# Optimization experiments

Hardware: AMD Instinct MI355X
Metric: run time of the kernel (lower is better)

The kernel has to match this reference:

```python
import jax, jax.numpy as jnp
import numpy as np

B, S, D, H = 2, 2048, 1024, 16
DK = D // H


def setup_inputs() -> dict:
    key = jax.random.key(0)
    ks = jax.random.split(key, 9)
    scale = 1.0 / np.sqrt(D)
    inp = {
        "x": jax.random.normal(ks[0], (B, S, D), dtype=jnp.float32),
        "mask": jnp.triu(jnp.ones((S, S), dtype=jnp.int32), k=1),  # 1 = masked (causal)
        "Wq": jax.random.normal(ks[1], (D, D), dtype=jnp.float32) * scale,
        "bq": jnp.zeros((D,), dtype=jnp.float32),
        "Wk": jax.random.normal(ks[2], (D, D), dtype=jnp.float32) * scale,
        "bk": jnp.zeros((D,), dtype=jnp.float32),
        "Wv": jax.random.normal(ks[3], (D, D), dtype=jnp.float32) * scale,
        "bv": jnp.zeros((D,), dtype=jnp.float32),
        "Wo": jax.random.normal(ks[4], (D, D), dtype=jnp.float32) * scale,
        "bo": jnp.zeros((D,), dtype=jnp.float32),
    }
    return inp


def reference(x, mask, Wq, bq, Wk, bk, Wv, bv, Wo, bo):
    # Linear projections (torch nn.Linear: x @ W.T + b; here W stored as (D, D) in
    # (in, out) layout so x @ W + b is equivalent math).
    q = x @ Wq + bq  # (B, S, D)
    k = x @ Wk + bk
    v = x @ Wv + bv
    # Split heads: (B, S, D) -> (B, H, S, DK)
    def split(t):
        return t.reshape(B, S, H, DK).transpose(0, 2, 1, 3)
    q, k, v = split(q), split(k), split(v)
    # Scaled dot-product attention with full score matrix (faithful to original)
    scores = jnp.einsum("bhsd,bhtd->bhst", q, k) / jnp.sqrt(jnp.float32(DK))
    scores = jnp.where(mask[None, None, :, :] == 1, -jnp.inf, scores)
    attn = jax.nn.softmax(scores, axis=-1)  # (B, H, S, S)
    out = jnp.einsum("bhst,bhtd->bhsd", attn, v)
    # Merge heads and final projection
    out = out.transpose(0, 2, 1, 3).reshape(B, S, D)
    return out @ Wo + bo
```

## Files before the change

kernel.cpp:

```cpp
#include <hip/hip_runtime.h>
#include <hip/hip_bf16.h>
#include <cstdint>
#include <cstddef>

typedef __attribute__((ext_vector_type(8))) short short8;
typedef __attribute__((ext_vector_type(4))) float f32x4;
typedef __attribute__((ext_vector_type(4))) unsigned int u32x4;
typedef unsigned short u16;
typedef unsigned int u32;

#define NB 2
#define NS 2048
#define ND 1024
#define NH 16
#define NDK 64

__device__ __forceinline__ u16 f2bf(float f){
  u32 u = __builtin_bit_cast(u32, f);
  u += 0x7fffu + ((u >> 16) & 1u);
  return (u16)(u >> 16);
}

__device__ __forceinline__ u32 pk2(float lo, float hi){
  return (u32)f2bf(lo) | ((u32)f2bf(hi) << 16);
}

__device__ __forceinline__ u32 cvtpk(float lo, float hi){
  u32 r;
  asm("v_cvt_pk_bf16_f32 %0, %1, %2" : "=v"(r) : "v"(lo), "v"(hi));
  return r;
}

__device__ __forceinline__ void stage16(const u16* g, u16* l, int lane){
#if defined(__has_builtin) && __has_builtin(__builtin_amdgcn_global_load_lds)
  __builtin_amdgcn_global_load_lds(
      (const __attribute__((address_space(1))) u32*)(const void*)g,
      (__attribute__((address_space(3))) u32*)(void*)l, 16, 0, 0);
#else
  ((uint4*)l)[lane] = *(const uint4*)g;
#endif
}


__global__ __launch_bounds__(256) void prep_kernel(
    const float* __restrict__ Wq, const float* __restrict__ Wk,
    const float* __restrict__ Wv, const float* __restrict__ Wo,
    const float* __restrict__ x,
    u16* __restrict__ Wt, u16* __restrict__ xb)
{
  const int z = blockIdx.z;
  const int tx = threadIdx.x, ty = threadIdx.y;
  if (z == 4){
    const int base = ((blockIdx.y*32 + (int)blockIdx.x)*256 + ty*32 + tx)*16;
    float4 v0 = *(const float4*)(x+base);
    float4 v1 = *(const float4*)(x+base+4);
    float4 v2 = *(const float4*)(x+base+8);
    float4 v3 = *(const float4*)(x+base+12);
    const int blk = base & ~31;
    const int h4  = (base & 16) ? 4 : 0;
    *(uint2*)(xb + blk +  0 + h4) = make_uint2(pk2(v0.x,v0.y), pk2(v0.z,v0.w));
    *(uint2*)(xb + blk +  8 + h4) = make_uint2(pk2(v1.x,v1.y), pk2(v1.z,v1.w));
    *(uint2*)(xb + blk + 16 + h4) = make_uint2(pk2(v2.x,v2.y), pk2(v2.z,v2.w));
    *(uint2*)(xb + blk + 24 + h4) = make_uint2(pk2(v3.x,v3.y), pk2(v3.z,v3.w));
    return;
  }
  const float* W = (z==0)?Wq:(z==1)?Wk:(z==2)?Wv:Wo;
  u16* dst = Wt + (size_t)z*ND*ND;
  __shared__ float t[32][33];
  const int n0 = blockIdx.x*32, k0 = blockIdx.y*32;
  const int ptx = 8*((tx&15)>>2) + (tx&3) + 4*(tx>>4);
#pragma unroll
  for (int i=0;i<4;i++) t[ty+i*8][tx] = W[(size_t)(k0+ty+i*8)*ND + n0+tx];
  __syncthreads();
#pragma unroll
  for (int i=0;i<4;i++) dst[(size_t)(n0+ty+i*8)*ND + k0+ptx] = f2bf(t[tx][ty+i*8]);
}

template<int MODE>
__global__ __launch_bounds__(256,3) void gemm_kernel(
    const u16* __restrict__ Abf, const u16* __restrict__ Wtz,
    const float* __restrict__ bias0, const float* __restrict__ bias1, const float* __restrict__ bias2,
    u16* __restrict__ Qout, u16* __restrict__ Kout, u16* __restrict__ Vtout,
    float* __restrict__ Fout)
{
  int bx, by;
  if constexpr (MODE==0){
    const int f  = blockIdx.x;
    const int fp = (f & 7)*96 + (f >> 3);
    by = fp / 24; bx = fp % 24;
  } else { bx = blockIdx.x; by = blockIdx.y; }
  const int tid  = threadIdx.x;
  const int lane = tid & 63;
  const int wv   = tid >> 6;
  const int a = lane & 15, g = lane >> 4;
  const int wm = wv >> 1, wn = wv & 1;
  const int m0 = by * 128, n0 = bx * 128;
  const int z  = (MODE==0) ? (n0 >> 10) : 0;

  __shared__ u16 Al[128*64];
  __shared__ u16 Bl[128*64];

  f32x4 acc[4][4] = {};

  const int grow = lane >> 3;
  const int gcol = (lane & 7) * 8;

#pragma unroll 1
  for (int k0 = 0; k0 < ND; k0 += 64) {
    __syncthreads();
#pragma unroll
    for (int i=0;i<4;++i){
      const int r = 32*wv + 8*i + grow;
      const int cs = gcol ^ ((r&7)<<3);
      stage16(Abf + (size_t)(m0+r)*ND + k0 + cs, &Al[(32*wv+8*i)*64], lane);
      stage16(Wtz + (size_t)(n0+r)*ND + k0 + cs, &Bl[(32*wv+8*i)*64], lane);
    }
    __syncthreads();

#pragma unroll
    for (int kk=0; kk<64; kk+=32){
      short8 af[4], bfr[4];
#pragma unroll
      for (int mi=0;mi<4;++mi){
        const int rr = wm*64 + mi*16 + a;
        const int rsw = (rr&7)<<3;
        af[mi] = *(const short8*)(&Al[rr*64] + ((kk + 8*g) ^ rsw));
      }
#pragma unroll
      for (int ni=0;ni<4;++ni){
        const int rr = wn*64 + ni*16 + a;
        const int rsw = (rr&7)<<3;
        bfr[ni] = *(const short8*)(&Bl[rr*64] + ((kk + 8*g) ^ rsw));
      }
      __builtin_amdgcn_s_setprio(1);
#pragma unroll
      for (int mi=0;mi<4;++mi)
#pragma unroll
        for (int ni=0;ni<4;++ni)
          acc[mi][ni] = __builtin_amdgcn_mfma_f32_16x16x32_bf16(af[mi], bfr[ni], acc[mi][ni], 0,0,0);
      __builtin_amdgcn_s_setprio(0);
    }
  }

#pragma unroll
  for (int mi=0;mi<4;++mi){
#pragma unroll
    for (int ni=0;ni<4;++ni){
      const int n  = n0 + wn*64 + ni*16 + a;
      const int mb = m0 + wm*64 + mi*16 + 4*g;
      if constexpr (MODE==0){
        const int nn = n & 1023;
        const float* bp = (z==0)? bias0 : (z==1)? bias1 : bias2;
        const float bias = bp[nn];
        const int h = nn >> 6, dk = nn & 63;
        const int b = mb >> 11, s = mb & 2047;
        if (z==2){
          const int sb = s & 31;
          const int col = (s & ~31) + 8*((sb&15)>>2) + 4*(sb>>4);
          *(uint2*)&Vtout[(((size_t)b*NH + h)*NDK + dk)*NS + col] =
            make_uint2(pk2(acc[mi][ni][0]+bias, acc[mi][ni][1]+bias),
                       pk2(acc[mi][ni][2]+bias, acc[mi][ni][3]+bias));
        } else {
          u16* dst = (z==0)? Qout : Kout;
          const float sc = (z==0)? 0.1803368801111601f : 1.0f;
          const int d5 = dk & 31;
          const int pdk = (dk & 32) + 8*((d5&15)>>2) + (d5&3) + 4*(d5>>4);
#pragma unroll
          for (int r=0;r<4;++r)
            dst[(((size_t)b*NH + h)*NS + (s+r))*NDK + pdk] = f2bf((acc[mi][ni][r]+bias)*sc);
        }
      } else {
        const float bias = bias0[n];
#pragma unroll
        for (int r=0;r<4;++r)
          Fout[(size_t)(mb+r)*ND + n] = acc[mi][ni][r] + bias;
      }
    }
  }
}

#define KOFF(p_, q_) ((p_)*8192 + (q_)*4096)
#define VOFF(p_, q_) (16384 + (p_)*8192 + (q_)*4096)
#define FIXM 10.0f

__global__ __launch_bounds__(512,4) void attn_kernel(
    const u16* __restrict__ Qg, const u16* __restrict__ Kg,
    const u16* __restrict__ Vtg, u16* __restrict__ Og)
{
  const int tid  = threadIdx.x;
  const int lane = tid & 63, wv = tid >> 6;
  const int qw = wv & 3, par = wv >> 2;
  const int a = lane & 15, g = lane >> 4;
  const int bh = blockIdx.x;
  const int qt = blockIdx.y;
  const int qb = (qt < 8) ? qt : (23 - qt);
  const int qB  = qb * 128;
  const int q0w = qB + qw*32;
  const int nr  = qb + 1;

  __shared__ u16 SH[32768];

  short8 qf[2][2];
#pragma unroll
  for (int qi=0; qi<2; ++qi){
    const u16* qptr = Qg + ((size_t)bh*NS + q0w + qi*16 + a)*NDK;
    qf[qi][0] = *(const short8*)(qptr + 8*g);
    qf[qi][1] = *(const short8*)(qptr + 32 + 8*g);
  }

  float ls[2] = {0.f, 0.f};
  f32x4 accO[4][2] = {};

  const int srow = wv*8 + (lane >> 3);
  const int scol = (lane & 7) * 8;
  const int scs  = scol ^ ((srow & 7) << 3);
  const u16* kgp = Kg  + (size_t)bh*NS*NDK + (size_t)srow*NDK + scs;
  const u16* vgp = Vtg + (size_t)bh*NDK*NS + (size_t)srow*NS  + scs;

  stage16(kgp,            &SH[KOFF(0,0) + wv*512], lane);
  stage16(kgp + 64*NDK,   &SH[KOFF(0,1) + wv*512], lane);
  stage16(vgp,            &SH[VOFF(0,0) + wv*512], lane);
  stage16(vgp + 64,       &SH[VOFF(0,1) + wv*512], lane);
  __syncthreads();

  const u16* kstg = kgp + 128*NDK;
  const u16* vstg = vgp + 128;

  int cur = 0;
#pragma unroll 1
  for (int r=0; r<nr; ++r){
    const int t = 2*r + par;
    const int kv0 = t * 64;
    if (r+1 < nr){
      stage16(kstg,          &SH[KOFF(cur^1,0) + wv*512], lane);
      stage16(kstg + 64*NDK, &SH[KOFF(cur^1,1) + wv*512], lane);
      stage16(vstg,          &SH[VOFF(cur^1,0) + wv*512], lane);
      stage16(vstg + 64,     &SH[VOFF(cur^1,1) + wv*512], lane);
      kstg += 128*NDK; vstg += 128;
    }

    if (kv0 <= q0w + 31){
      const u16* Kb = &SH[KOFF(cur,par)];
      const u16* Vb = &SH[VOFF(cur,par)];
      f32x4 sc[2][4] = {};
      __builtin_amdgcn_s_setprio(1);
#pragma unroll
      for (int kvf=0; kvf<4; ++kvf){
        const int rr = kvf*16 + a;
        const int rsw = (rr&7)<<3;
        const u16* rp = Kb + rr*64;
        short8 kf0 = *(const short8*)(rp + ((8*g) ^ rsw));
        short8 kf1 = *(const short8*)(rp + ((32 + 8*g) ^ rsw));
#pragma unroll
        for (int qi=0; qi<2; ++qi){
          sc[qi][kvf] = __builtin_amdgcn_mfma_f32_16x16x32_bf16(kf0, qf[qi][0], sc[qi][kvf], 0,0,0);
          sc[qi][kvf] = __builtin_amdgcn_mfma_f32_16x16x32_bf16(kf1, qf[qi][1], sc[qi][kvf], 0,0,0);
        }
      }
      __builtin_amdgcn_s_setprio(0);

      const bool dm = (kv0 + 63 > q0w);
      short8 pf[2][2];
#pragma unroll
      for (int qi=0; qi<2; ++qi){
        const int q = q0w + qi*16 + a;
        if (dm){
#pragma unroll
          for (int kvf=0;kvf<4;++kvf)
#pragma unroll
            for (int rr=0;rr<4;++rr){
              const int kv = kv0 + kvf*16 + 4*g + rr;
              if (kv > q) sc[qi][kvf][rr] = -1e30f;
            }
        }
        float rsum = 0.f;
        u32 pw[2][4];
#pragma unroll
        for (int kvf=0;kvf<4;++kvf){
          const float e0 = exp2f(sc[qi][kvf][0] - FIXM);
          const float e1 = exp2f(sc[qi][kvf][1] - FIXM);
          const float e2 = exp2f(sc[qi][kvf][2] - FIXM);
          const float e3 = exp2f(sc[qi][kvf][3] - FIXM);
          rsum += (e0+e1)+(e2+e3);
          pw[kvf>>1][(kvf&1)*2+0] = cvtpk(e0,e1);
          pw[kvf>>1][(kvf&1)*2+1] = cvtpk(e2,e3);
        }
        pf[qi][0] = __builtin_bit_cast(short8, *(u32x4*)pw[0]);
        pf[qi][1] = __builtin_bit_cast(short8, *(u32x4*)pw[1]);
        rsum += __shfl_xor(rsum,16);
        rsum += __shfl_xor(rsum,32);
        ls[qi] += rsum;
      }

      __builtin_amdgcn_s_setprio(1);
#pragma unroll
      for (int dkg=0;dkg<4;++dkg){
        const int rr = dkg*16 + a;
        const int rsw = (rr&7)<<3;
        const u16* rp = Vb + rr*64;
        short8 vf0 = *(const short8*)(rp + ((8*g) ^ rsw));
        short8 vf1 = *(const short8*)(rp + ((32 + 8*g) ^ rsw));
#pragma unroll
        for (int qi=0; qi<2; ++qi){
          accO[dkg][qi] = __builtin_amdgcn_mfma_f32_16x16x32_bf16(vf0, pf[qi][0], accO[dkg][qi], 0,0,0);
          accO[dkg][qi] = __builtin_amdgcn_mfma_f32_16x16x32_bf16(vf1, pf[qi][1], accO[dkg][qi], 0,0,0);
        }
      }
      __builtin_amdgcn_s_setprio(0);
    }

    __syncthreads();
    cur ^= 1;
  }

  float* ms = (float*)SH;
  if (par == 1){
#pragma unroll
    for (int qi=0; qi<2; ++qi){
      const int idx = (((qw*64 + lane)*2) + qi)*17;
#pragma unroll
      for (int dkg=0;dkg<4;++dkg)
#pragma unroll
        for (int j=0;j<4;++j) ms[idx + dkg*4 + j] = accO[dkg][qi][j];
      ms[idx+16] = ls[qi];
    }
  }
  __syncthreads();

  if (par == 0){
    u16* Lw = &SH[18432] + qw*2048;
#pragma unroll
    for (int qi=0; qi<2; ++qi){
      const int idx = (((qw*64 + lane)*2) + qi)*17;
      const float linv = 1.0f / (ls[qi] + ms[idx+16]);
      const int row = qi*16 + a;
#pragma unroll
      for (int dkg=0; dkg<4; ++dkg){
        const int pcol = 32*(dkg>>1) + 8*g + 4*(dkg&1);
        const float o0 = (accO[dkg][qi][0] + ms[idx+dkg*4+0])*linv;
        const float o1 = (accO[dkg][qi][1] + ms[idx+dkg*4+1])*linv;
        const float o2 = (accO[dkg][qi][2] + ms[idx+dkg*4+2])*linv;
        const float o3 = (accO[dkg][qi][3] + ms[idx+dkg*4+3])*linv;
        *(uint2*)&Lw[(row<<6) + (pcol ^ ((row&7)<<3))] = make_uint2(cvtpk(o0,o1), cvtpk(o2,o3));
      }
    }
    const int b = bh >> 4, h = bh & 15;
#pragma unroll
    for (int j=0; j<4; ++j){
      const int row = j*8 + (lane>>3);
      const int cc  = (lane&7)*8;
      uint4 d = *(const uint4*)&Lw[(row<<6) + (cc ^ ((row&7)<<3))];
      *(uint4*)(Og + ((size_t)b*NS + qB + qw*32 + row)*ND + h*NDK + cc) = d;
    }
  }
}

extern "C" void kernel_launch(void* const* d_in, const int* in_sizes, int n_in,
                              void* d_out, int out_size, void* d_ws, size_t ws_size,
                              hipStream_t stream) {
  (void)in_sizes; (void)n_in; (void)out_size; (void)ws_size;
  const float* x  = (const float*)d_in[0];
  const float* Wq = (const float*)d_in[2];
  const float* bq = (const float*)d_in[3];
  const float* Wk = (const float*)d_in[4];
  const float* bk = (const float*)d_in[5];
  const float* Wv = (const float*)d_in[6];
  const float* bv = (const float*)d_in[7];
  const float* Wo = (const float*)d_in[8];
  const float* bo = (const float*)d_in[9];
  float* out = (float*)d_out;

  u16* Wt  = (u16*)d_ws;
  u16* Qb  = Wt  + (size_t)4194304;
  u16* Kb  = Qb  + (size_t)4194304;
  u16* Vtb = Kb  + (size_t)4194304;
  u16* XO  = Vtb + (size_t)4194304;

  prep_kernel<<<dim3(32,32,5), dim3(32,8,1), 0, stream>>>(Wq, Wk, Wv, Wo, x, Wt, XO);
  gemm_kernel<0><<<dim3(768), dim3(256), 0, stream>>>(
      XO, Wt, bq, bk, bv, Qb, Kb, Vtb, (float*)nullptr);
  attn_kernel<<<dim3(32,16), dim3(512), 0, stream>>>(Qb, Kb, Vtb, XO);
  gemm_kernel<1><<<dim3(8,32), dim3(256), 0, stream>>>(
      XO, Wt + (size_t)3*1048576, bo, nullptr, nullptr,
      (u16*)nullptr, (u16*)nullptr, (u16*)nullptr, out);
}
```

Baseline: 107.2 us.

## Drop KV-parity wave split in attention; use 4-wave blocks over all KV tiles

```diff
diff --git a/kernel.cpp b/kernel.cpp
--- a/kernel.cpp
+++ b/kernel.cpp
@@ -179,26 +179,24 @@
   }
 }
 
-#define KOFF(p_, q_) ((p_)*8192 + (q_)*4096)
-#define VOFF(p_, q_) (16384 + (p_)*8192 + (q_)*4096)
+#define KOFF(p_) ((p_)*4096)
+#define VOFF(p_) (8192 + (p_)*4096)
 #define FIXM 10.0f
 
-__global__ __launch_bounds__(512,4) void attn_kernel(
+__global__ __launch_bounds__(256,4) void attn_kernel(
     const u16* __restrict__ Qg, const u16* __restrict__ Kg,
     const u16* __restrict__ Vtg, u16* __restrict__ Og)
 {
   const int tid  = threadIdx.x;
   const int lane = tid & 63, wv = tid >> 6;
-  const int qw = wv & 3, par = wv >> 2;
   const int a = lane & 15, g = lane >> 4;
   const int bh = blockIdx.x;
-  const int qt = blockIdx.y;
-  const int qb = (qt < 8) ? qt : (23 - qt);
+  const int qb = 15 - (int)blockIdx.y;
   const int qB  = qb * 128;
-  const int q0w = qB + qw*32;
-  const int nr  = qb + 1;
-
-  __shared__ u16 SH[32768];
+  const int q0w = qB + wv*32;
+  const int nt  = 2*qb + 2;
+
+  __shared__ u16 SH[16384];
 
   short8 qf[2][2];
 #pragma unroll
@@ -211,37 +209,39 @@
   float ls[2] = {0.f, 0.f};
   f32x4 accO[4][2] = {};
 
-  const int srow = wv*8 + (lane >> 3);
+  const int srow = wv*16 + (lane >> 3);
   const int scol = (lane & 7) * 8;
   const int scs  = scol ^ ((srow & 7) << 3);
   const u16* kgp = Kg  + (size_t)bh*NS*NDK + (size_t)srow*NDK + scs;
   const u16* vgp = Vtg + (size_t)bh*NDK*NS + (size_t)srow*NS  + scs;
-
-  stage16(kgp,            &SH[KOFF(0,0) + wv*512], lane);
-  stage16(kgp + 64*NDK,   &SH[KOFF(0,1) + wv*512], lane);
-  stage16(vgp,            &SH[VOFF(0,0) + wv*512], lane);
-  stage16(vgp + 64,       &SH[VOFF(0,1) + wv*512], lane);
+  u16* const kd0 = &SH[(wv*16)*64];
+  u16* const kd1 = &SH[(wv*16+8)*64];
+
+  stage16(kgp,          kd0,        lane);
+  stage16(kgp + 8*NDK,  kd1,        lane);
+  stage16(vgp,          kd0 + 8192, lane);
+  stage16(vgp + 8*NS,   kd1 + 8192, lane);
   __syncthreads();
 
-  const u16* kstg = kgp + 128*NDK;
-  const u16* vstg = vgp + 128;
+  const u16* kstg = kgp + 64*NDK;
+  const u16* vstg = vgp + 64;
 
   int cur = 0;
 #pragma unroll 1
-  for (int r=0; r<nr; ++r){
-    const int t = 2*r + par;
+  for (int t=0; t<nt; ++t){
     const int kv0 = t * 64;
-    if (r+1 < nr){
-      stage16(kstg,          &SH[KOFF(cur^1,0) + wv*512], lane);
-      stage16(kstg + 64*NDK, &SH[KOFF(cur^1,1) + wv*512], lane);
-      stage16(vstg,          &SH[VOFF(cur^1,0) + wv*512], lane);
-      stage16(vstg + 64,     &SH[VOFF(cur^1,1) + wv*512], lane);
-      kstg += 128*NDK; vstg += 128;
+    if (t+1 < nt){
+      const int nb = (cur^1)*4096;
+      stage16(kstg,          kd0 + nb,        lane);
+      stage16(kstg + 8*NDK,  kd1 + nb,        lane);
+      stage16(vstg,          kd0 + nb + 8192, lane);
+      stage16(vstg + 8*NS,   kd1 + nb + 8192, lane);
+      kstg += 64*NDK; vstg += 64;
     }
 
     if (kv0 <= q0w + 31){
-      const u16* Kb = &SH[KOFF(cur,par)];
-      const u16* Vb = &SH[VOFF(cur,par)];
+      const u16* Kb = &SH[KOFF(cur)];
+      const u16* Vb = &SH[VOFF(cur)];
       f32x4 sc[2][4] = {};
       __builtin_amdgcn_s_setprio(1);
 #pragma unroll
@@ -313,45 +313,28 @@
     cur ^= 1;
   }
 
-  float* ms = (float*)SH;
-  if (par == 1){
-#pragma unroll
-    for (int qi=0; qi<2; ++qi){
-      const int idx = (((qw*64 + lane)*2) + qi)*17;
-#pragma unroll
-      for (int dkg=0;dkg<4;++dkg)
-#pragma unroll
-        for (int j=0;j<4;++j) ms[idx + dkg*4 + j] = accO[dkg][qi][j];
-      ms[idx+16] = ls[qi];
-    }
-  }
-  __syncthreads();
-
-  if (par == 0){
-    u16* Lw = &SH[18432] + qw*2048;
-#pragma unroll
-    for (int qi=0; qi<2; ++qi){
-      const int idx = (((qw*64 + lane)*2) + qi)*17;
-      const float linv = 1.0f / (ls[qi] + ms[idx+16]);
-      const int row = qi*16 + a;
-#pragma unroll
-      for (int dkg=0; dkg<4; ++dkg){
-        const int pcol = 32*(dkg>>1) + 8*g + 4*(dkg&1);
-        const float o0 = (accO[dkg][qi][0] + ms[idx+dkg*4+0])*linv;
-        const float o1 = (accO[dkg][qi][1] + ms[idx+dkg*4+1])*linv;
-        const float o2 = (accO[dkg][qi][2] + ms[idx+dkg*4+2])*linv;
-        const float o3 = (accO[dkg][qi][3] + ms[idx+dkg*4+3])*linv;
-        *(uint2*)&Lw[(row<<6) + (pcol ^ ((row&7)<<3))] = make_uint2(cvtpk(o0,o1), cvtpk(o2,o3));
-      }
-    }
-    const int b = bh >> 4, h = bh & 15;
-#pragma unroll
-    for (int j=0; j<4; ++j){
-      const int row = j*8 + (lane>>3);
-      const int cc  = (lane&7)*8;
-      uint4 d = *(const uint4*)&Lw[(row<<6) + (cc ^ ((row&7)<<3))];
-      *(uint4*)(Og + ((size_t)b*NS + qB + qw*32 + row)*ND + h*NDK + cc) = d;
-    }
+  u16* Lw = &SH[0] + wv*2048;
+#pragma unroll
+  for (int qi=0; qi<2; ++qi){
+    const float linv = 1.0f / ls[qi];
+    const int row = qi*16 + a;
+#pragma unroll
+    for (int dkg=0; dkg<4; ++dkg){
+      const int pcol = 32*(dkg>>1) + 8*g + 4*(dkg&1);
+      const float o0 = accO[dkg][qi][0]*linv;
+      const float o1 = accO[dkg][qi][1]*linv;
+      const float o2 = accO[dkg][qi][2]*linv;
+      const float o3 = accO[dkg][qi][3]*linv;
+      *(uint2*)&Lw[(row<<6) + (pcol ^ ((row&7)<<3))] = make_uint2(cvtpk(o0,o1), cvtpk(o2,o3));
+    }
+  }
+  const int b = bh >> 4, h = bh & 15;
+#pragma unroll
+  for (int j=0; j<4; ++j){
+    const int row = j*8 + (lane>>3);
+    const int cc  = (lane&7)*8;
+    uint4 d = *(const uint4*)&Lw[(row<<6) + (cc ^ ((row&7)<<3))];
+    *(uint4*)(Og + ((size_t)b*NS + qB + wv*32 + row)*ND + h*NDK + cc) = d;
   }
 }
 
@@ -379,7 +362,7 @@
   prep_kernel<<<dim3(32,32,5), dim3(32,8,1), 0, stream>>>(Wq, Wk, Wv, Wo, x, Wt, XO);
   gemm_kernel<0><<<dim3(768), dim3(256), 0, stream>>>(
       XO, Wt, bq, bk, bv, Qb, Kb, Vtb, (float*)nullptr);
-  attn_kernel<<<dim3(32,16), dim3(512), 0, stream>>>(Qb, Kb, Vtb, XO);
+  attn_kernel<<<dim3(32,16), dim3(256), 0, stream>>>(Qb, Kb, Vtb, XO);
   gemm_kernel<1><<<dim3(8,32), dim3(256), 0, stream>>>(
       XO, Wt + (size_t)3*1048576, bo, nullptr, nullptr,
       (u16*)nullptr, (u16*)nullptr, (u16*)nullptr, out);
```

New measurement: 116.2 us. 1.08x slower.
